# Kernel optimization log

Hardware: AMD Instinct MI355X
Metric: run time of the kernel (lower is better)

## Reference

```python
import jax, jax.numpy as jnp
from jax import lax
import numpy as np

N, C, H, W = 8, 256, 96, 96
K = 5            # d_conv=4 forced odd -> 5 in FauxScan1D
HID = 2 * C      # ff_mult * dim


def setup_inputs() -> dict:
    key = jax.random.key(0)
    ks = iter(jax.random.split(key, 40))
    nrm = lambda *s: jax.random.normal(next(ks), s, jnp.float32) * 0.02
    inp = {'x': jax.random.normal(next(ks), (N, C, H, W), jnp.float32)}
    inp['ln1_w'] = jnp.ones((C,), jnp.float32)
    inp['ln1_b'] = jnp.zeros((C,), jnp.float32)
    inp['dw_w'] = nrm(3, 3, 1, C)   # depthwise 3x3, HWIO with feature_group_count=C
    inp['dw_b'] = jnp.zeros((C,), jnp.float32)
    for d in ('lr', 'rl', 'tb', 'bt'):
        inp[d + '_dw_w'] = nrm(K, 1, C)   # depthwise conv1d, WIO
        inp[d + '_dw_b'] = jnp.zeros((C,), jnp.float32)
        inp[d + '_g_w'] = nrm(C, C)       # 1x1 gate conv (out, in)
        inp[d + '_g_b'] = jnp.zeros((C,), jnp.float32)
    inp['fuse_w'] = nrm(C, C)
    inp['fuse_b'] = jnp.zeros((C,), jnp.float32)
    inp['ln2_w'] = jnp.ones((C,), jnp.float32)
    inp['ln2_b'] = jnp.zeros((C,), jnp.float32)
    inp['ff1_w'] = nrm(2 * HID, C)
    inp['ff1_b'] = jnp.zeros((2 * HID,), jnp.float32)
    inp['ff2_w'] = nrm(C, HID)
    inp['ff2_b'] = jnp.zeros((C,), jnp.float32)
    return inp


def _ln2d(x, w, b, eps=1e-6):
    # LayerNorm2d: per-(sample, channel) stats over H,W
    m = x.mean(axis=(2, 3), keepdims=True)
    v = ((x - m) ** 2).mean(axis=(2, 3), keepdims=True)
    return (x - m) * lax.rsqrt(v + eps) * w[None, :, None, None] + b[None, :, None, None]


def _scan1d(seq, dw_w, dw_b, g_w, g_b):
    # FauxScan1D: seq (B, L, C) -> dwconv1d(k=5, pad=2) * sigmoid(pointwise gate)
    c = seq.shape[-1]
    y = lax.conv_general_dilated(seq, dw_w, (1,), [(K // 2, K // 2)],
                                 dimension_numbers=('NWC', 'WIO', 'NWC'),
                                 feature_group_count=c) + dw_b
    g = jax.nn.sigmoid(jnp.einsum('blc,dc->bld', seq, g_w) + g_b)
    return y * g


def _forward(x, ln1_w, ln1_b, dw_w, dw_b,
             lr_dw_w, lr_dw_b, lr_g_w, lr_g_b,
             rl_dw_w, rl_dw_b, rl_g_w, rl_g_b,
             tb_dw_w, tb_dw_b, tb_g_w, tb_g_b,
             bt_dw_w, bt_dw_b, bt_g_w, bt_g_b,
             fuse_w, fuse_b, ln2_w, ln2_b, ff1_w, ff1_b, ff2_w, ff2_b):
    n, c, hh, ww = x.shape
    y = _ln2d(x, ln1_w, ln1_b)
    y = lax.conv_general_dilated(y, dw_w, (1, 1), [(1, 1), (1, 1)],
                                 dimension_numbers=('NCHW', 'HWIO', 'NCHW'),
                                 feature_group_count=c) + dw_b[None, :, None, None]
    y = jnp.transpose(y, (0, 2, 3, 1))  # NHWC
    # lr: rows as sequences
    o = _scan1d(y.reshape(n * hh, ww, c), lr_dw_w, lr_dw_b, lr_g_w, lr_g_b).reshape(n, hh, ww, c)
    # rl: flip width, scan, flip back
    yf = jnp.flip(y, 2).reshape(n * hh, ww, c)
    o = o + jnp.flip(_scan1d(yf, rl_dw_w, rl_dw_b, rl_g_w, rl_g_b).reshape(n, hh, ww, c), 2)
    # tb: columns as sequences
    yt = jnp.transpose(y, (0, 2, 1, 3)).reshape(n * ww, hh, c)
    o = o + jnp.transpose(_scan1d(yt, tb_dw_w, tb_dw_b, tb_g_w, tb_g_b).reshape(n, ww, hh, c), (0, 2, 1, 3))
    # bt: flip height, columns, scan, undo
    yb = jnp.transpose(jnp.flip(y, 1), (0, 2, 1, 3)).reshape(n * ww, hh, c)
    o = o + jnp.flip(jnp.transpose(_scan1d(yb, bt_dw_w, bt_dw_b, bt_g_w, bt_g_b).reshape(n, ww, hh, c), (0, 2, 1, 3)), 1)
    y = jnp.transpose(o, (0, 3, 1, 2))  # back to NCHW
    y = jnp.einsum('nchw,dc->ndhw', y, fuse_w) + fuse_b[None, :, None, None]
    x = x + y
    z = _ln2d(x, ln2_w, ln2_b)
    z = jnp.einsum('nchw,dc->ndhw', z, ff1_w) + ff1_b[None, :, None, None]
    a, g = jnp.split(z, 2, axis=1)  # GLU on channel dim
    z = a * jax.nn.sigmoid(g)
    z = jnp.einsum('nchw,dc->ndhw', z, ff2_w) + ff2_b[None, :, None, None]
    return x + z


def reference(x, ln1_w, ln1_b, dw_w, dw_b,
              lr_dw_w, lr_dw_b, lr_g_w, lr_g_b,
              rl_dw_w, rl_dw_b, rl_g_w, rl_g_b,
              tb_dw_w, tb_dw_b, tb_g_w, tb_g_b,
              bt_dw_w, bt_dw_b, bt_g_w, bt_g_b,
              fuse_w, fuse_b, ln2_w, ln2_b, ff1_w, ff1_b, ff2_w, ff2_b):
    return _forward(x, ln1_w, ln1_b, dw_w, dw_b,
                    lr_dw_w, lr_dw_b, lr_g_w, lr_g_b,
                    rl_dw_w, rl_dw_b, rl_g_w, rl_g_b,
                    tb_dw_w, tb_dw_b, tb_g_w, tb_g_b,
                    bt_dw_w, bt_dw_b, bt_g_w, bt_g_b,
                    fuse_w, fuse_b, ln2_w, ln2_b, ff1_w, ff1_b, ff2_w, ff2_b)
```

## Files before the change

kernel.cpp:

```cpp
#include <hip/hip_runtime.h>

#define TPB 256
#define HWSZ 9216
#define RS 528
#define RS2 272

typedef __attribute__((ext_vector_type(8))) short short8x;
typedef __attribute__((ext_vector_type(4))) float f32x4;
typedef unsigned short ushort_t;
typedef unsigned int uint_t;

__device__ __forceinline__ float sigf(float v) { return 1.0f / (1.0f + __expf(-v)); }

__device__ __forceinline__ ushort_t f2bf(float f) {
  __bf16 h = (__bf16)f;
  return __builtin_bit_cast(ushort_t, h);
}
__device__ __forceinline__ float bf2f(ushort_t h) {
  return __uint_as_float(((uint_t)h) << 16);
}

__global__ __launch_bounds__(TPB) void k_pack(
    const float* __restrict__ lrg, const float* __restrict__ rlg,
    const float* __restrict__ tbg, const float* __restrict__ btg,
    const float* __restrict__ fusew, const float* __restrict__ ff1w,
    const float* __restrict__ ff2w,
    ushort_t* __restrict__ Gp, ushort_t* __restrict__ Ftp,
    ushort_t* __restrict__ W1p, ushort_t* __restrict__ W2p) {
  int i = blockIdx.x * TPB + threadIdx.x;
  if (i < 262144) {
    int d = i >> 16, r = i & 65535;
    int kt = r >> 13, nt = (r >> 9) & 15, l = (r >> 3) & 63, j = r & 7;
    int k = kt * 32 + (l >> 4) * 8 + j;
    int n_ = nt * 16 + (l & 15);
    const float* g = (d == 0) ? lrg : (d == 1) ? rlg : (d == 2) ? tbg : btg;
    Gp[i] = f2bf(g[n_ * 256 + k]);
  } else if (i < 327680) {
    int r = i - 262144;
    int kt = r >> 13, nt = (r >> 9) & 15, l = (r >> 3) & 63, j = r & 7;
    int k = kt * 32 + (l >> 4) * 8 + j;
    int n_ = nt * 16 + (l & 15);
    Ftp[r] = f2bf(fusew[n_ * 256 + k]);
  } else if (i < 589824) {
    int r = i - 327680;
    int kt = r >> 15, pb = (r >> 10) & 31, ag = (r >> 9) & 1;
    int l = (r >> 3) & 63, j = r & 7;
    int k = kt * 32 + (l >> 4) * 8 + j;
    int colb = pb * 16 + (l & 15);
    int col = ag ? (512 + colb) : colb;
    W1p[r] = f2bf(ff1w[col * 256 + k]);
  } else if (i < 720896) {
    int r = i - 589824;
    int kt = r >> 13, nt = (r >> 9) & 15, l = (r >> 3) & 63, j = r & 7;
    int k = kt * 32 + (l >> 4) * 8 + j;
    int n_ = nt * 16 + (l & 15);
    W2p[r] = f2bf(ff2w[n_ * 512 + k]);
  }
}

__global__ __launch_bounds__(TPB) void k_stats(const float* __restrict__ src,
                                               float* __restrict__ mean,
                                               float* __restrict__ rstd) {
  int nc = blockIdx.x;
  const float4* p = (const float4*)(src + (long)nc * HWSZ);
  float s = 0.f, s2 = 0.f;
  for (int i = threadIdx.x; i < 2304; i += TPB) {
    float4 v = p[i];
    s += (v.x + v.y) + (v.z + v.w);
    s2 = fmaf(v.x, v.x, fmaf(v.y, v.y, fmaf(v.z, v.z, fmaf(v.w, v.w, s2))));
  }
#pragma unroll
  for (int off = 32; off > 0; off >>= 1) {
    s += __shfl_down(s, off);
    s2 += __shfl_down(s2, off);
  }
  __shared__ float ls[4], ls2[4];
  int lane = threadIdx.x & 63, wv = threadIdx.x >> 6;
  if (lane == 0) { ls[wv] = s; ls2[wv] = s2; }
  __syncthreads();
  if (threadIdx.x == 0) {
    float S = ls[0] + ls[1] + ls[2] + ls[3];
    float S2 = ls2[0] + ls2[1] + ls2[2] + ls2[3];
    float m = S * (1.0f / HWSZ);
    float var = S2 * (1.0f / HWSZ) - m * m;
    mean[nc] = m;
    rstd[nc] = rsqrtf(fmaxf(var, 0.f) + 1e-6f);
  }
}

__global__ __launch_bounds__(TPB) void k_lndw(
    const float* __restrict__ x, const float* __restrict__ mean1,
    const float* __restrict__ rstd1, const float* __restrict__ ln1w,
    const float* __restrict__ ln1b, const float* __restrict__ dww,
    const float* __restrict__ dwb, ushort_t* __restrict__ y,
    ushort_t* __restrict__ yT) {
  __shared__ __align__(16) ushort_t xs[6 * 32 * 104];
  __shared__ __align__(16) ushort_t ot[2 * 96 * 32];
  __shared__ float sc[32], sh[32];

  int tid = threadIdx.x;
  int bid = blockIdx.x;
  int cb = (bid & 7) * 32;
  int hb = (bid >> 3) % 24;
  int n  = bid / 192;
  int h0 = hb * 4;

  if (tid < 32) {
    int c = cb + tid;
    int nc = n * 256 + c;
    float scale = rstd1[nc] * ln1w[c];
    sc[tid] = scale;
    sh[tid] = ln1b[c] - mean1[nc] * scale;
  }
  if (tid < 192) {
    xs[tid * 104 + 3] = 0;
    xs[tid * 104 + 100] = 0;
  }
  __syncthreads();

  for (int i = tid; i < 4608; i += TPB) {
    int rc = i / 24;
    int f4 = i - rc * 24;
    int row = rc >> 5, c = rc & 31;
    int hh = h0 - 1 + row;
    uint2 pk = make_uint2(0, 0);
    if (hh >= 0 && hh < 96) {
      float4 v = *(const float4*)(x + (long)(n * 256 + cb + c) * HWSZ +
                                  hh * 96 + f4 * 4);
      float scale = sc[c], shift = sh[c];
      ushort_t p0 = f2bf(fmaf(v.x, scale, shift));
      ushort_t p1 = f2bf(fmaf(v.y, scale, shift));
      ushort_t p2 = f2bf(fmaf(v.z, scale, shift));
      ushort_t p3 = f2bf(fmaf(v.w, scale, shift));
      pk.x = (uint_t)p0 | ((uint_t)p1 << 16);
      pk.y = (uint_t)p2 | ((uint_t)p3 << 16);
    }
    *(uint2*)(xs + rc * 104 + 4 + f4 * 4) = pk;
  }
  __syncthreads();

  int c = tid & 31, grp = tid >> 5;
  int w0 = grp * 12;
  float wgt[9];
#pragma unroll
  for (int t = 0; t < 9; ++t) wgt[t] = dww[t * 256 + cb + c];
  float bias = dwb[cb + c];

#pragma unroll
  for (int half = 0; half < 2; ++half) {
    float vals[2][12];
#pragma unroll
    for (int sub = 0; sub < 2; ++sub) {
      int orow = half * 2 + sub;
      float R[3][14];
#pragma unroll
      for (int rr = 0; rr < 3; ++rr) {
        const ushort_t* p = xs + ((orow + rr) * 32 + c) * 104;
        R[rr][0] = bf2f(p[3 + w0]);
        ushort4 q0 = *(const ushort4*)(p + 4 + w0);
        ushort4 q1 = *(const ushort4*)(p + 8 + w0);
        ushort4 q2 = *(const ushort4*)(p + 12 + w0);
        R[rr][1] = bf2f(q0.x);  R[rr][2] = bf2f(q0.y);
        R[rr][3] = bf2f(q0.z);  R[rr][4] = bf2f(q0.w);
        R[rr][5] = bf2f(q1.x);  R[rr][6] = bf2f(q1.y);
        R[rr][7] = bf2f(q1.z);  R[rr][8] = bf2f(q1.w);
        R[rr][9] = bf2f(q2.x);  R[rr][10] = bf2f(q2.y);
        R[rr][11] = bf2f(q2.z); R[rr][12] = bf2f(q2.w);
        R[rr][13] = bf2f(p[16 + w0]);
      }
#pragma unroll
      for (int k = 0; k < 12; ++k) {
        float acc = bias;
#pragma unroll
        for (int rr = 0; rr < 3; ++rr) {
          acc = fmaf(R[rr][k], wgt[rr * 3 + 0], acc);
          acc = fmaf(R[rr][k + 1], wgt[rr * 3 + 1], acc);
          acc = fmaf(R[rr][k + 2], wgt[rr * 3 + 2], acc);
        }
        vals[sub][k] = acc;
      }
    }
    if (half == 1) __syncthreads();
#pragma unroll
    for (int sub = 0; sub < 2; ++sub)
#pragma unroll
      for (int k = 0; k < 12; ++k)
        ot[(sub * 96 + w0 + k) * 32 + c] = f2bf(vals[sub][k]);
    __syncthreads();
#pragma unroll
    for (int it = 0; it < 3; ++it) {
      int u = it * 256 + tid;
      int r2 = (u >= 384) ? 1 : 0;
      int rem = u - r2 * 384;
      int w = rem >> 2, cq = rem & 3;
      uint4 v = *(const uint4*)(ot + (r2 * 96 + w) * 32 + cq * 8);
      int h = h0 + half * 2 + r2;
      *(uint4*)(y + ((long)(n * 96 + h) * 96 + w) * 256 + cb + cq * 8) = v;
      *(uint4*)(yT + ((long)(n * 96 + w) * 96 + h) * 256 + cb + cq * 8) = v;
    }
  }
}

__global__ __launch_bounds__(512, 4) void k_scan(
    const ushort_t* __restrict__ src, const uint4* __restrict__ gp4,
    const float* __restrict__ dwaw, const float* __restrict__ dwab,
    const float* __restrict__ gab, const float* __restrict__ dwbw,
    const float* __restrict__ dwbb, const float* __restrict__ gbb,
    ushort_t* __restrict__ dst) {
  __shared__ __align__(16) char pool[52 * RS + 16 * RS];
  char* ylds = pool;
  char* olds = pool + 52 * RS;

  int tid = threadIdx.x;
  int bid = blockIdx.x;
  int seg = bid & 1, line = (bid >> 1) % 96, n = bid / 192;
  int p0 = seg * 48;
  long lbase = (long)(n * 96 + line) * 96;

  for (int u = tid; u < 52 * 32; u += 512) {
    int r = u >> 5, ks = u & 31;
    int q = p0 - 2 + r;
    uint4 v = make_uint4(0, 0, 0, 0);
    if (q >= 0 && q < 96)
      v = *(const uint4*)(src + (lbase + q) * 256 + ks * 8);
    *(uint4*)(ylds + r * RS + ks * 16) = v;
  }
  __syncthreads();

  int l = tid & 63, w = tid >> 6;
  int llo = l & 15, lhi = l >> 4;

  float part[3][2][4];

#pragma unroll
  for (int diri = 0; diri < 2; ++diri) {
    f32x4 acc[3][2];
#pragma unroll
    for (int mf = 0; mf < 3; ++mf)
#pragma unroll
      for (int ntl = 0; ntl < 2; ++ntl) acc[mf][ntl] = (f32x4){0.f, 0.f, 0.f, 0.f};

    const uint4* gbase = gp4 + ((long)(diri * 8) * 16 + w * 2) * 64 + l;
    short8x bc0 = *(const short8x*)(gbase);
    short8x bc1 = *(const short8x*)(gbase + 64);
#pragma unroll
    for (int kt = 0; kt < 8; ++kt) {
      short8x bn0, bn1;
      if (kt < 7) {
        bn0 = *(const short8x*)(gbase + (kt + 1) * 1024);
        bn1 = *(const short8x*)(gbase + (kt + 1) * 1024 + 64);
      }
      short8x a[3];
#pragma unroll
      for (int mf = 0; mf < 3; ++mf) {
        int arow = 2 + mf * 16 + llo;
        a[mf] = *(const short8x*)(ylds + arow * RS + kt * 64 + lhi * 16);
      }
#pragma unroll
      for (int mf = 0; mf < 3; ++mf) {
        acc[mf][0] = __builtin_amdgcn_mfma_f32_16x16x32_bf16(a[mf], bc0, acc[mf][0], 0, 0, 0);
        acc[mf][1] = __builtin_amdgcn_mfma_f32_16x16x32_bf16(a[mf], bc1, acc[mf][1], 0, 0, 0);
      }
      bc0 = bn0;
      bc1 = bn1;
    }

    const float* dwv = diri ? dwbw : dwaw;
    const float* dbv = diri ? dwbb : dwab;
    const float* gbv = diri ? gbb : gab;
#pragma unroll
    for (int ntl = 0; ntl < 2; ++ntl) {
      int c = (w * 2 + ntl) * 16 + llo;
      float wt[5];
#pragma unroll
      for (int t = 0; t < 5; ++t)
        wt[t] = diri ? dwv[(4 - t) * 256 + c] : dwv[t * 256 + c];
      float cb = dbv[c], gb = gbv[c];
#pragma unroll
      for (int mf = 0; mf < 3; ++mf) {
        int pbase = mf * 16 + lhi * 4;
        float yv[8];
#pragma unroll
        for (int t = 0; t < 8; ++t) {
          int ry = pbase + t;
          yv[t] = bf2f(*(const ushort_t*)(ylds + ry * RS + c * 2));
        }
#pragma unroll
        for (int r = 0; r < 4; ++r) {
          float conv = cb;
#pragma unroll
          for (int t = 0; t < 5; ++t) conv = fmaf(yv[r + t], wt[t], conv);
          float val = conv * sigf(acc[mf][ntl][r] + gb);
          if (diri == 0) part[mf][ntl][r] = val;
          else           part[mf][ntl][r] += val;
        }
      }
    }
  }

#pragma unroll
  for (int mf = 0; mf < 3; ++mf) {
    __syncthreads();
#pragma unroll
    for (int ntl = 0; ntl < 2; ++ntl) {
      int c = (w * 2 + ntl) * 16 + llo;
#pragma unroll
      for (int r = 0; r < 4; ++r) {
        int p = lhi * 4 + r;
        *(ushort_t*)(olds + p * RS + c * 2) = f2bf(part[mf][ntl][r]);
      }
    }
    __syncthreads();
    {
      int p = tid >> 5, ks = tid & 31;
      uint4 v = *(const uint4*)(olds + p * RS + ks * 16);
      *(uint4*)(dst + (lbase + p0 + mf * 16 + p) * 256 + ks * 8) = v;
    }
  }
}

__global__ __launch_bounds__(512, 4) void k_fuse(
    const ushort_t* __restrict__ o, const ushort_t* __restrict__ oT,
    const ushort_t* __restrict__ Ftp, const float* __restrict__ fuseb,
    const float* __restrict__ x, float* __restrict__ out,
    float* __restrict__ sumb, float* __restrict__ sqb) {
  __shared__ __align__(16) char pool[48 * RS];

  int tid = threadIdx.x;
  int pix0 = blockIdx.x * 48;
  int n = pix0 / HWSZ, hw0 = pix0 % HWSZ;
  int h = hw0 / 96, w0 = hw0 % 96;

  for (int u = tid; u < 48 * 32; u += 512) {
    int r = u >> 5, ks = u & 31;
    uint4 va = *(const uint4*)(o + (long)(pix0 + r) * 256 + ks * 8);
    uint4 vb = *(const uint4*)(oT + ((long)(n * 96 + w0 + r) * 96 + h) * 256 + ks * 8);
    ushort_t* a8 = (ushort_t*)&va;
    ushort_t* b8 = (ushort_t*)&vb;
#pragma unroll
    for (int j = 0; j < 8; ++j) a8[j] = f2bf(bf2f(a8[j]) + bf2f(b8[j]));
    *(uint4*)(pool + r * RS + ks * 16) = va;
  }
  __syncthreads();

  int l = tid & 63, w = tid >> 6;
  int llo = l & 15, lhi = l >> 4;

  const uint4* fp4 = (const uint4*)Ftp;
  f32x4 acc[3][2];
#pragma unroll
  for (int mf = 0; mf < 3; ++mf)
#pragma unroll
    for (int ntl = 0; ntl < 2; ++ntl) acc[mf][ntl] = (f32x4){0.f, 0.f, 0.f, 0.f};

  const uint4* fbase = fp4 + (long)(w * 2) * 64 + l;
  short8x bc0 = *(const short8x*)(fbase);
  short8x bc1 = *(const short8x*)(fbase + 64);
#pragma unroll
  for (int kt = 0; kt < 8; ++kt) {
    short8x bn0, bn1;
    if (kt < 7) {
      bn0 = *(const short8x*)(fbase + (kt + 1) * 1024);
      bn1 = *(const short8x*)(fbase + (kt + 1) * 1024 + 64);
    }
    short8x a[3];
#pragma unroll
    for (int mf = 0; mf < 3; ++mf) {
      int arow = mf * 16 + llo;
      a[mf] = *(const short8x*)(pool + arow * RS + kt * 64 + lhi * 16);
    }
#pragma unroll
    for (int mf = 0; mf < 3; ++mf) {
      acc[mf][0] = __builtin_amdgcn_mfma_f32_16x16x32_bf16(a[mf], bc0, acc[mf][0], 0, 0, 0);
      acc[mf][1] = __builtin_amdgcn_mfma_f32_16x16x32_bf16(a[mf], bc1, acc[mf][1], 0, 0, 0);
    }
    bc0 = bn0;
    bc1 = bn1;
  }

  float s1[2] = {0.f, 0.f}, s2[2] = {0.f, 0.f};
#pragma unroll
  for (int mf = 0; mf < 3; ++mf)
#pragma unroll
    for (int ntl = 0; ntl < 2; ++ntl) {
      int c = (w * 2 + ntl) * 16 + llo;
      float fb = fuseb[c];
      long addr = (long)(n * 256 + c) * HWSZ + hw0 + mf * 16 + lhi * 4;
      float4 xv = *(const float4*)(x + addr);
      float4 ov;
      ov.x = xv.x + acc[mf][ntl][0] + fb;
      ov.y = xv.y + acc[mf][ntl][1] + fb;
      ov.z = xv.z + acc[mf][ntl][2] + fb;
      ov.w = xv.w + acc[mf][ntl][3] + fb;
      *(float4*)(out + addr) = ov;
      s1[ntl] += (ov.x + ov.y) + (ov.z + ov.w);
      s2[ntl] += fmaf(ov.x, ov.x, fmaf(ov.y, ov.y, fmaf(ov.z, ov.z, ov.w * ov.w)));
    }
#pragma unroll
  for (int ntl = 0; ntl < 2; ++ntl) {
    s1[ntl] += __shfl_xor(s1[ntl], 16);
    s2[ntl] += __shfl_xor(s2[ntl], 16);
    s1[ntl] += __shfl_xor(s1[ntl], 32);
    s2[ntl] += __shfl_xor(s2[ntl], 32);
  }
  if (lhi == 0) {
#pragma unroll
    for (int ntl = 0; ntl < 2; ++ntl) {
      int c = (w * 2 + ntl) * 16 + llo;
      atomicAdd(&sumb[n * 256 + c], s1[ntl]);
      atomicAdd(&sqb[n * 256 + c], s2[ntl]);
    }
  }
}

__global__ __launch_bounds__(512, 4) void k_ff1(
    const float* __restrict__ xres, const float* __restrict__ sumb,
    const float* __restrict__ sqb, const float* __restrict__ ln2w,
    const float* __restrict__ ln2b, const ushort_t* __restrict__ W1p,
    const float* __restrict__ ff1b, ushort_t* __restrict__ u) {
  __shared__ __align__(16) char hA[96 * RS];
  __shared__ float sc[256], sh[256];

  int tid = threadIdx.x;
  int pix0 = blockIdx.x * 96;
  int n = pix0 / HWSZ, hw0 = pix0 % HWSZ;

  if (tid < 256) {
    int nc = n * 256 + tid;
    float m = sumb[nc] * (1.0f / HWSZ);
    float var = sqb[nc] * (1.0f / HWSZ) - m * m;
    float rstd = rsqrtf(fmaxf(var, 0.f) + 1e-6f);
    float scale = rstd * ln2w[tid];
    sc[tid] = scale;
    sh[tid] = ln2b[tid] - m * scale;
  }
  __syncthreads();

  for (int i = tid; i < 6144; i += 512) {
    int cp = i / 48, pp = i % 48;
    int c0 = cp * 2;
    long base0 = (long)(n * 256 + c0) * HWSZ + hw0 + pp * 2;
    float2 v0 = *(const float2*)(xres + base0);
    float2 v1 = *(const float2*)(xres + base0 + HWSZ);
    float s0 = sc[c0], h0 = sh[c0];
    float s1 = sc[c0 + 1], h1 = sh[c0 + 1];
    int p0 = pp * 2;
    uint_t w0 = (uint_t)f2bf(fmaf(v0.x, s0, h0)) |
                ((uint_t)f2bf(fmaf(v1.x, s1, h1)) << 16);
    uint_t w1 = (uint_t)f2bf(fmaf(v0.y, s0, h0)) |
                ((uint_t)f2bf(fmaf(v1.y, s1, h1)) << 16);
    *(uint_t*)(hA + p0 * RS + c0 * 2) = w0;
    *(uint_t*)(hA + (p0 + 1) * RS + c0 * 2) = w1;
  }
  __syncthreads();

  int l = tid & 63, w = tid >> 6;
  int llo = l & 15, lhi = l >> 4;

  const uint4* W1p4 = (const uint4*)W1p;
#pragma unroll
  for (int q = 0; q < 4; ++q) {
    int pb = q * 8 + w;
    f32x4 ca[6][2];
#pragma unroll
    for (int mf = 0; mf < 6; ++mf) {
      ca[mf][0] = (f32x4){0.f, 0.f, 0.f, 0.f};
      ca[mf][1] = (f32x4){0.f, 0.f, 0.f, 0.f};
    }
    const uint4* wb = W1p4 + (long)(pb * 2) * 64 + l;
    short8x bca = *(const short8x*)(wb);
    short8x bcg = *(const short8x*)(wb + 64);
#pragma unroll
    for (int kt = 0; kt < 8; ++kt) {
      short8x bna, bng;
      if (kt < 7) {
        bna = *(const short8x*)(wb + (kt + 1) * 4096);
        bng = *(const short8x*)(wb + (kt + 1) * 4096 + 64);
      }
      short8x a[6];
#pragma unroll
      for (int mf = 0; mf < 6; ++mf) {
        int arow = mf * 16 + llo;
        a[mf] = *(const short8x*)(hA + arow * RS + kt * 64 + lhi * 16);
      }
#pragma unroll
      for (int mf = 0; mf < 6; ++mf) {
        ca[mf][0] = __builtin_amdgcn_mfma_f32_16x16x32_bf16(a[mf], bca, ca[mf][0], 0, 0, 0);
        ca[mf][1] = __builtin_amdgcn_mfma_f32_16x16x32_bf16(a[mf], bcg, ca[mf][1], 0, 0, 0);
      }
      bca = bna;
      bcg = bng;
    }
    int ucol = pb * 16 + llo;
    float ba = ff1b[ucol], bg = ff1b[512 + ucol];
    int rb0 = (pix0 >> 2) + lhi;
#pragma unroll
    for (int mf = 0; mf < 6; ++mf) {
      ushort_t b0 = f2bf((ca[mf][0][0] + ba) * sigf(ca[mf][1][0] + bg));
      ushort_t b1 = f2bf((ca[mf][0][1] + ba) * sigf(ca[mf][1][1] + bg));
      ushort_t b2 = f2bf((ca[mf][0][2] + ba) * sigf(ca[mf][1][2] + bg));
      ushort_t b3 = f2bf((ca[mf][0][3] + ba) * sigf(ca[mf][1][3] + bg));
      uint2 pk;
      pk.x = (uint_t)b0 | ((uint_t)b1 << 16);
      pk.y = (uint_t)b2 | ((uint_t)b3 << 16);
      *(uint2*)(u + ((long)(rb0 + mf * 4) * 512 + ucol) * 4) = pk;
    }
  }
}

__global__ __launch_bounds__(512, 4) void k_ff2(
    const ushort_t* __restrict__ u, const ushort_t* __restrict__ W2p,
    const float* __restrict__ ff2b, float* __restrict__ out) {
  __shared__ __align__(16) char pool[96 * RS2];

  int tid = threadIdx.x;
  int pix0 = blockIdx.x * 96;
  int n = pix0 / HWSZ, hw0 = pix0 % HWSZ;
  int rb0 = pix0 >> 2;

  int l = tid & 63, w = tid >> 6;
  int llo = l & 15, lhi = l >> 4;

  const uint4* W2p4 = (const uint4*)W2p;

  uint2 st[6];
#pragma unroll
  for (int t = 0; t < 6; ++t) {
    int i = t * 512 + tid;
    int col = i & 127, rbl = i >> 7;
    st[t] = *(const uint2*)(u + ((long)(rb0 + rbl) * 512 + col) * 4);
  }

  f32x4 zacc[6][2];
#pragma unroll
  for (int mf = 0; mf < 6; ++mf) {
    zacc[mf][0] = (f32x4){0.f, 0.f, 0.f, 0.f};
    zacc[mf][1] = (f32x4){0.f, 0.f, 0.f, 0.f};
  }

#pragma unroll
  for (int kc = 0; kc < 4; ++kc) {
    if (kc) __syncthreads();
#pragma unroll
    for (int t = 0; t < 6; ++t) {
      int i = t * 512 + tid;
      int col = i & 127, rbl = i >> 7;
      int p = rbl * 4;
      ushort_t* b = (ushort_t*)&st[t];
#pragma unroll
      for (int k = 0; k < 4; ++k)
        *(ushort_t*)(pool + (p + k) * RS2 + col * 2) = b[k];
    }
    __syncthreads();
    if (kc < 3) {
#pragma unroll
      for (int t = 0; t < 6; ++t) {
        int i = t * 512 + tid;
        int col = i & 127, rbl = i >> 7;
        st[t] = *(const uint2*)(u + ((long)(rb0 + rbl) * 512 + (kc + 1) * 128 + col) * 4);
      }
    }
#pragma unroll
    for (int ks = 0; ks < 4; ++ks) {
      int kt = kc * 4 + ks;
      short8x a[6];
#pragma unroll
      for (int mf = 0; mf < 6; ++mf) {
        int arow = mf * 16 + llo;
        a[mf] = *(const short8x*)(pool + arow * RS2 + ks * 64 + lhi * 16);
      }
      short8x b0 = *(const short8x*)(W2p4 + (long)(kt * 16 + w * 2) * 64 + l);
      short8x b1 = *(const short8x*)(W2p4 + (long)(kt * 16 + w * 2 + 1) * 64 + l);
#pragma unroll
      for (int mf = 0; mf < 6; ++mf) {
        zacc[mf][0] = __builtin_amdgcn_mfma_f32_16x16x32_bf16(a[mf], b0, zacc[mf][0], 0, 0, 0);
        zacc[mf][1] = __builtin_amdgcn_mfma_f32_16x16x32_bf16(a[mf], b1, zacc[mf][1], 0, 0, 0);
      }
    }
  }

#pragma unroll
  for (int mf = 0; mf < 6; ++mf)
#pragma unroll
    for (int ntl = 0; ntl < 2; ++ntl) {
      int c = (w * 2 + ntl) * 16 + llo;
      float fb = ff2b[c];
      long addr = (long)(n * 256 + c) * HWSZ + hw0 + mf * 16 + lhi * 4;
      float4 ov = *(const float4*)(out + addr);
      ov.x += zacc[mf][ntl][0] + fb;
      ov.y += zacc[mf][ntl][1] + fb;
      ov.z += zacc[mf][ntl][2] + fb;
      ov.w += zacc[mf][ntl][3] + fb;
      *(float4*)(out + addr) = ov;
    }
}

extern "C" void kernel_launch(void* const* d_in, const int* in_sizes, int n_in,
                              void* d_out, int out_size, void* d_ws, size_t ws_size,
                              hipStream_t stream) {
  (void)in_sizes; (void)n_in; (void)out_size; (void)ws_size;
  const float* x     = (const float*)d_in[0];
  const float* ln1w  = (const float*)d_in[1];
  const float* ln1b  = (const float*)d_in[2];
  const float* dww   = (const float*)d_in[3];
  const float* dwb   = (const float*)d_in[4];
  const float* lr_w  = (const float*)d_in[5];
  const float* lr_b  = (const float*)d_in[6];
  const float* lr_gw = (const float*)d_in[7];
  const float* lr_gb = (const float*)d_in[8];
  const float* rl_w  = (const float*)d_in[9];
  const float* rl_b  = (const float*)d_in[10];
  const float* rl_gw = (const float*)d_in[11];
  const float* rl_gb = (const float*)d_in[12];
  const float* tb_w  = (const float*)d_in[13];
  const float* tb_b  = (const float*)d_in[14];
  const float* tb_gw = (const float*)d_in[15];
  const float* tb_gb = (const float*)d_in[16];
  const float* bt_w  = (const float*)d_in[17];
  const float* bt_b  = (const float*)d_in[18];
  const float* bt_gw = (const float*)d_in[19];
  const float* bt_gb = (const float*)d_in[20];
  const float* fusew = (const float*)d_in[21];
  const float* fuseb = (const float*)d_in[22];
  const float* ln2w  = (const float*)d_in[23];
  const float* ln2b  = (const float*)d_in[24];
  const float* ff1w  = (const float*)d_in[25];
  const float* ff1b  = (const float*)d_in[26];
  const float* ff2w  = (const float*)d_in[27];
  const float* ff2b  = (const float*)d_in[28];

  float* out = (float*)d_out;
  ushort_t* y  = (ushort_t*)d_ws;
  ushort_t* yT = y + 18874368;
  ushort_t* o  = yT + 18874368;
  ushort_t* oT = o + 18874368;
  ushort_t* uu = y;
  float* mean1 = (float*)(oT + 18874368);
  float* rstd1 = mean1 + 2048;
  float* sumb  = rstd1 + 2048;
  float* sqb   = sumb + 2048;
  ushort_t* Gp  = (ushort_t*)(sqb + 2048);
  ushort_t* Ftp = Gp + 262144;
  ushort_t* W1p = Ftp + 65536;
  ushort_t* W2p = W1p + 262144;

  hipMemsetAsync(sumb, 0, 4096 * sizeof(float), stream);
  k_pack<<<2816, TPB, 0, stream>>>(lr_gw, rl_gw, tb_gw, bt_gw, fusew, ff1w, ff2w,
                                   Gp, Ftp, W1p, W2p);
  k_stats<<<2048, TPB, 0, stream>>>(x, mean1, rstd1);
  k_lndw<<<1536, TPB, 0, stream>>>(x, mean1, rstd1, ln1w, ln1b, dww, dwb, y, yT);
  k_scan<<<1536, 512, 0, stream>>>(y, (const uint4*)Gp,
                                   lr_w, lr_b, lr_gb, rl_w, rl_b, rl_gb, o);
  k_scan<<<1536, 512, 0, stream>>>(yT, (const uint4*)(Gp + 131072),
                                   tb_w, tb_b, tb_gb, bt_w, bt_b, bt_gb, oT);
  k_fuse<<<1536, 512, 0, stream>>>(o, oT, Ftp, fuseb, x, out, sumb, sqb);
  k_ff1<<<768, 512, 0, stream>>>(out, sumb, sqb, ln2w, ln2b, W1p, ff1b, uu);
  k_ff2<<<768, 512, 0, stream>>>(uu, W2p, ff2b, out);
}
```

Measured before the change: 316.8 us.

## Fuse FF1 GLU and FF2 GEMMs into one kernel via LDS chunks

Merges k_ff1 and k_ff2 into a single kernel. Each 128-wide chunk of the GLU output is written to a shared-memory buffer and immediately consumed by the FF2 MFMA accumulation, so the bf16 hidden tensor no longer round-trips through global memory. The cost is two extra block barriers per chunk, more LDS per block (which may lower occupancy), and the loss of the explicit register prefetch of W1 tiles.

Result: slower. 362.6 us (+14.5%).

```diff
diff --git a/kernel.cpp b/kernel.cpp
--- a/kernel.cpp
+++ b/kernel.cpp
@@ -413,12 +413,14 @@
   }
 }
 
-__global__ __launch_bounds__(512, 4) void k_ff1(
+__global__ __launch_bounds__(512, 4) void k_ff(
     const float* __restrict__ xres, const float* __restrict__ sumb,
     const float* __restrict__ sqb, const float* __restrict__ ln2w,
     const float* __restrict__ ln2b, const ushort_t* __restrict__ W1p,
-    const float* __restrict__ ff1b, ushort_t* __restrict__ u) {
+    const float* __restrict__ ff1b, const ushort_t* __restrict__ W2p,
+    const float* __restrict__ ff2b, float* __restrict__ out) {
   __shared__ __align__(16) char hA[96 * RS];
+  __shared__ __align__(16) char uC[96 * RS2];
   __shared__ float sc[256], sh[256];
 
   int tid = threadIdx.x;
@@ -458,7 +460,15 @@
   int llo = l & 15, lhi = l >> 4;
 
   const uint4* W1p4 = (const uint4*)W1p;
-#pragma unroll
+  const uint4* W2p4 = (const uint4*)W2p;
+
+  f32x4 zacc[6][2];
+#pragma unroll
+  for (int mf = 0; mf < 6; ++mf) {
+    zacc[mf][0] = (f32x4){0.f, 0.f, 0.f, 0.f};
+    zacc[mf][1] = (f32x4){0.f, 0.f, 0.f, 0.f};
+  }
+
   for (int q = 0; q < 4; ++q) {
     int pb = q * 8 + w;
     f32x4 ca[6][2];
@@ -468,113 +478,44 @@
       ca[mf][1] = (f32x4){0.f, 0.f, 0.f, 0.f};
     }
     const uint4* wb = W1p4 + (long)(pb * 2) * 64 + l;
-    short8x bca = *(const short8x*)(wb);
-    short8x bcg = *(const short8x*)(wb + 64);
 #pragma unroll
     for (int kt = 0; kt < 8; ++kt) {
-      short8x bna, bng;
-      if (kt < 7) {
-        bna = *(const short8x*)(wb + (kt + 1) * 4096);
-        bng = *(const short8x*)(wb + (kt + 1) * 4096 + 64);
-      }
-      short8x a[6];
+      short8x bca = *(const short8x*)(wb + (long)kt * 4096);
+      short8x bcg = *(const short8x*)(wb + (long)kt * 4096 + 64);
 #pragma unroll
       for (int mf = 0; mf < 6; ++mf) {
-        int arow = mf * 16 + llo;
-        a[mf] = *(const short8x*)(hA + arow * RS + kt * 64 + lhi * 16);
-      }
-#pragma unroll
-      for (int mf = 0; mf < 6; ++mf) {
-        ca[mf][0] = __builtin_amdgcn_mfma_f32_16x16x32_bf16(a[mf], bca, ca[mf][0], 0, 0, 0);
-        ca[mf][1] = __builtin_amdgcn_mfma_f32_16x16x32_bf16(a[mf], bcg, ca[mf][1], 0, 0, 0);
-      }
-      bca = bna;
-      bcg = bng;
-    }
-    int ucol = pb * 16 + llo;
-    float ba = ff1b[ucol], bg = ff1b[512 + ucol];
-    int rb0 = (pix0 >> 2) + lhi;
-#pragma unroll
-    for (int mf = 0; mf < 6; ++mf) {
-      ushort_t b0 = f2bf((ca[mf][0][0] + ba) * sigf(ca[mf][1][0] + bg));
-      ushort_t b1 = f2bf((ca[mf][0][1] + ba) * sigf(ca[mf][1][1] + bg));
-      ushort_t b2 = f2bf((ca[mf][0][2] + ba) * sigf(ca[mf][1][2] + bg));
-      ushort_t b3 = f2bf((ca[mf][0][3] + ba) * sigf(ca[mf][1][3] + bg));
-      uint2 pk;
-      pk.x = (uint_t)b0 | ((uint_t)b1 << 16);
-      pk.y = (uint_t)b2 | ((uint_t)b3 << 16);
-      *(uint2*)(u + ((long)(rb0 + mf * 4) * 512 + ucol) * 4) = pk;
-    }
-  }
-}
-
-__global__ __launch_bounds__(512, 4) void k_ff2(
-    const ushort_t* __restrict__ u, const ushort_t* __restrict__ W2p,
-    const float* __restrict__ ff2b, float* __restrict__ out) {
-  __shared__ __align__(16) char pool[96 * RS2];
-
-  int tid = threadIdx.x;
-  int pix0 = blockIdx.x * 96;
-  int n = pix0 / HWSZ, hw0 = pix0 % HWSZ;
-  int rb0 = pix0 >> 2;
-
-  int l = tid & 63, w = tid >> 6;
-  int llo = l & 15, lhi = l >> 4;
-
-  const uint4* W2p4 = (const uint4*)W2p;
-
-  uint2 st[6];
-#pragma unroll
-  for (int t = 0; t < 6; ++t) {
-    int i = t * 512 + tid;
-    int col = i & 127, rbl = i >> 7;
-    st[t] = *(const uint2*)(u + ((long)(rb0 + rbl) * 512 + col) * 4);
-  }
-
-  f32x4 zacc[6][2];
-#pragma unroll
-  for (int mf = 0; mf < 6; ++mf) {
-    zacc[mf][0] = (f32x4){0.f, 0.f, 0.f, 0.f};
-    zacc[mf][1] = (f32x4){0.f, 0.f, 0.f, 0.f};
-  }
-
-#pragma unroll
-  for (int kc = 0; kc < 4; ++kc) {
-    if (kc) __syncthreads();
-#pragma unroll
-    for (int t = 0; t < 6; ++t) {
-      int i = t * 512 + tid;
-      int col = i & 127, rbl = i >> 7;
-      int p = rbl * 4;
-      ushort_t* b = (ushort_t*)&st[t];
-#pragma unroll
-      for (int k = 0; k < 4; ++k)
-        *(ushort_t*)(pool + (p + k) * RS2 + col * 2) = b[k];
-    }
+        short8x a = *(const short8x*)(hA + (mf * 16 + llo) * RS + kt * 64 + lhi * 16);
+        ca[mf][0] = __builtin_amdgcn_mfma_f32_16x16x32_bf16(a, bca, ca[mf][0], 0, 0, 0);
+        ca[mf][1] = __builtin_amdgcn_mfma_f32_16x16x32_bf16(a, bcg, ca[mf][1], 0, 0, 0);
+      }
+    }
+
     __syncthreads();
-    if (kc < 3) {
-#pragma unroll
-      for (int t = 0; t < 6; ++t) {
-        int i = t * 512 + tid;
-        int col = i & 127, rbl = i >> 7;
-        st[t] = *(const uint2*)(u + ((long)(rb0 + rbl) * 512 + (kc + 1) * 128 + col) * 4);
-      }
-    }
+    {
+      int ucol = pb * 16 + llo;
+      int lcol = w * 16 + llo;
+      float ba = ff1b[ucol], bg = ff1b[512 + ucol];
+#pragma unroll
+      for (int mf = 0; mf < 6; ++mf)
+#pragma unroll
+        for (int r = 0; r < 4; ++r) {
+          int p = mf * 16 + lhi * 4 + r;
+          float uv = (ca[mf][0][r] + ba) * sigf(ca[mf][1][r] + bg);
+          *(ushort_t*)(uC + p * RS2 + lcol * 2) = f2bf(uv);
+        }
+    }
+    __syncthreads();
+
 #pragma unroll
     for (int ks = 0; ks < 4; ++ks) {
-      int kt = kc * 4 + ks;
-      short8x a[6];
-#pragma unroll
-      for (int mf = 0; mf < 6; ++mf) {
-        int arow = mf * 16 + llo;
-        a[mf] = *(const short8x*)(pool + arow * RS2 + ks * 64 + lhi * 16);
-      }
+      int kt = q * 4 + ks;
       short8x b0 = *(const short8x*)(W2p4 + (long)(kt * 16 + w * 2) * 64 + l);
       short8x b1 = *(const short8x*)(W2p4 + (long)(kt * 16 + w * 2 + 1) * 64 + l);
 #pragma unroll
       for (int mf = 0; mf < 6; ++mf) {
-        zacc[mf][0] = __builtin_amdgcn_mfma_f32_16x16x32_bf16(a[mf], b0, zacc[mf][0], 0, 0, 0);
-        zacc[mf][1] = __builtin_amdgcn_mfma_f32_16x16x32_bf16(a[mf], b1, zacc[mf][1], 0, 0, 0);
+        short8x a2 = *(const short8x*)(uC + (mf * 16 + llo) * RS2 + ks * 64 + lhi * 16);
+        zacc[mf][0] = __builtin_amdgcn_mfma_f32_16x16x32_bf16(a2, b0, zacc[mf][0], 0, 0, 0);
+        zacc[mf][1] = __builtin_amdgcn_mfma_f32_16x16x32_bf16(a2, b1, zacc[mf][1], 0, 0, 0);
       }
     }
   }
@@ -634,7 +575,6 @@
   ushort_t* yT = y + 18874368;
   ushort_t* o  = yT + 18874368;
   ushort_t* oT = o + 18874368;
-  ushort_t* uu = y;
   float* mean1 = (float*)(oT + 18874368);
   float* rstd1 = mean1 + 2048;
   float* sumb  = rstd1 + 2048;
@@ -654,6 +594,6 @@
   k_scan<<<1536, 512, 0, stream>>>(yT, (const uint4*)(Gp + 131072),
                                    tb_w, tb_b, tb_gb, bt_w, bt_b, bt_gb, oT);
   k_fuse<<<1536, 512, 0, stream>>>(o, oT, Ftp, fuseb, x, out, sumb, sqb);
-  k_ff1<<<768, 512, 0, stream>>>(out, sumb, sqb, ln2w, ln2b, W1p, ff1b, uu);
-  k_ff2<<<768, 512, 0, stream>>>(uu, W2p, ff2b, out);
-}
+  k_ff<<<768, 512, 0, stream>>>(out, sumb, sqb, ln2w, ln2b, W1p, ff1b,
+                                W2p, ff2b, out);
+}
```
